# Optimization experiments

Hardware: AMD Instinct MI355X
Metric: run time of the kernel (lower is better)

Reference implementation:

```python
import jax, jax.numpy as jnp
import numpy as np

B, K, D = 32768, 8192, 1024
DECAY = 0.99
EPS = 1e-05
COMMIT = 0.25
NORM_EPS = 1e-12  # matches F.normalize eps


def _l2norm(x):
    n = jnp.linalg.norm(x, axis=-1, keepdims=True)
    return x / jnp.maximum(n, NORM_EPS)


def setup_inputs() -> dict:
    key = jax.random.key(0)
    k1, k2 = jax.random.split(key)
    z = jax.random.normal(k1, (B, D), jnp.float32)
    codebook = _l2norm(jax.random.normal(k2, (K, D), jnp.float32))
    ema_count = jnp.zeros((K,), jnp.float32)
    ema_weight = codebook  # init: ema_weight = codebook.clone()
    return {"z": z, "codebook": codebook, "ema_count": ema_count, "ema_weight": ema_weight}


def reference(z, codebook, ema_count, ema_weight):
    # cosine-similarity nearest-codeword search
    z_norm = _l2norm(z)                      # [B, D]
    cb_norm = _l2norm(codebook)              # [K, D]
    sim = jnp.einsum('bd,kd->bk', z_norm, cb_norm)  # [B, K]
    code_ids = jnp.argmax(sim, axis=-1)      # [B]
    q = codebook[code_ids]                   # [B, D] gather

    # EMA codebook update (training-mode statistics, no grad)
    zs = jax.lax.stop_gradient(z)
    n_k = jax.ops.segment_sum(jnp.ones((B,), z.dtype), code_ids, num_segments=K)  # [K]
    sum_k = jax.ops.segment_sum(zs, code_ids, num_segments=K)                      # [K, D]
    new_count = DECAY * ema_count + (1.0 - DECAY) * n_k
    new_weight = DECAY * ema_weight + (1.0 - DECAY) * sum_k
    new_codebook = new_weight / (new_count[:, None] + EPS)

    # commitment loss + straight-through estimator
    loss = COMMIT * jnp.mean((z - jax.lax.stop_gradient(q)) ** 2)
    z_q = z + jax.lax.stop_gradient(q - z)
    return z_q, code_ids, loss, new_codebook, new_count, new_weight
```

## Files before the change

kernel.cpp:

```cpp
#include <hip/hip_runtime.h>
#include <hip/hip_bf16.h>
#include <cstdint>
#include <cstddef>


#define B_N 32768
#define K_N 8192
#define D_N 1024
#define DECAYF 0.99f
#define OMDECAYF 0.01f
#define EPSF 1e-5f
#define NORM_EPSF 1e-12f

#define BT 128
#define KT 128
#define DT 32
#define LDT 40
#define NKT (K_N / KT)

typedef _Float16 f16x8 __attribute__((ext_vector_type(8)));
typedef _Float16 f16x4 __attribute__((ext_vector_type(4)));
typedef float f32x4 __attribute__((ext_vector_type(4)));

__global__ __launch_bounds__(256) void row_scale_kernel(
    const float* __restrict__ x, float* __restrict__ scale) {
  const int row = blockIdx.x;
  const float4 v =
      reinterpret_cast<const float4*>(x + (size_t)row * D_N)[threadIdx.x];
  float ss = v.x * v.x + v.y * v.y + v.z * v.z + v.w * v.w;
  for (int off = 32; off; off >>= 1) ss += __shfl_down(ss, off, 64);
  __shared__ float w[4];
  const int lane = threadIdx.x & 63, wid = threadIdx.x >> 6;
  if (lane == 0) w[wid] = ss;
  __syncthreads();
  if (threadIdx.x == 0) {
    const float t = w[0] + w[1] + w[2] + w[3];
    scale[row] = 64.0f / fmaxf(sqrtf(t), NORM_EPSF);
  }
}

__global__ __launch_bounds__(256) void gemm_argmax_kernel(
    const float* __restrict__ z, const float* __restrict__ cb,
    const float* __restrict__ scaleA, const float* __restrict__ scaleB,
    float* __restrict__ pval, int* __restrict__ pidx) {
  __shared__ _Float16 sAh[BT * LDT];
  __shared__ _Float16 sAl[BT * LDT];
  __shared__ _Float16 sBh[KT * LDT];
  __shared__ _Float16 sBl[KT * LDT];
  __shared__ float sSA[BT];
  __shared__ float sSB[KT];
  __shared__ float smv[BT][2];
  __shared__ int smc[BT][2];

  const int tid = threadIdx.x;
  const int kt = blockIdx.x & (NKT - 1);
  const int bt = blockIdx.x >> 6;
  const int b0 = bt * BT;
  const int k0 = kt * KT;

  if (tid < 128) sSA[tid] = scaleA[b0 + tid];
  else           sSB[tid - 128] = scaleB[k0 + tid - 128];
  __syncthreads();

  const int lane = tid & 63;
  const int q = lane >> 4;
  const int ln = lane & 15;
  const int wid = tid >> 6;
  const int wm = wid >> 1;
  const int wn = wid & 1;

  f32x4 acc[4][4];
#pragma unroll
  for (int i = 0; i < 4; ++i)
#pragma unroll
    for (int j = 0; j < 4; ++j) acc[i][j] = (f32x4){0.f, 0.f, 0.f, 0.f};

  for (int it = 0; it < D_N / DT; ++it) {
    const int d0 = it * DT;
#pragma unroll
    for (int c = 0; c < 4; ++c) {
      const int ch = tid + c * 256;
      const int row = ch >> 3;
      const int seg = (ch & 7) << 2;
      {
        float4 v = *reinterpret_cast<const float4*>(
            z + (size_t)(b0 + row) * D_N + d0 + seg);
        const float s = sSA[row];
        const float x0 = v.x * s, x1 = v.y * s, x2 = v.z * s, x3 = v.w * s;
        f16x4 h, l;
        h[0] = (_Float16)x0; l[0] = (_Float16)(x0 - (float)h[0]);
        h[1] = (_Float16)x1; l[1] = (_Float16)(x1 - (float)h[1]);
        h[2] = (_Float16)x2; l[2] = (_Float16)(x2 - (float)h[2]);
        h[3] = (_Float16)x3; l[3] = (_Float16)(x3 - (float)h[3]);
        *reinterpret_cast<f16x4*>(&sAh[row * LDT + seg]) = h;
        *reinterpret_cast<f16x4*>(&sAl[row * LDT + seg]) = l;
      }
      {
        float4 v = *reinterpret_cast<const float4*>(
            cb + (size_t)(k0 + row) * D_N + d0 + seg);
        const float s = sSB[row];
        const float x0 = v.x * s, x1 = v.y * s, x2 = v.z * s, x3 = v.w * s;
        f16x4 h, l;
        h[0] = (_Float16)x0; l[0] = (_Float16)(x0 - (float)h[0]);
        h[1] = (_Float16)x1; l[1] = (_Float16)(x1 - (float)h[1]);
        h[2] = (_Float16)x2; l[2] = (_Float16)(x2 - (float)h[2]);
        h[3] = (_Float16)x3; l[3] = (_Float16)(x3 - (float)h[3]);
        *reinterpret_cast<f16x4*>(&sBh[row * LDT + seg]) = h;
        *reinterpret_cast<f16x4*>(&sBl[row * LDT + seg]) = l;
      }
    }
    __syncthreads();

    f16x8 ah[4], al[4], bh[4], bl[4];
#pragma unroll
    for (int i = 0; i < 4; ++i) {
      const int r = wm * 64 + i * 16 + ln;
      ah[i] = *reinterpret_cast<const f16x8*>(&sAh[r * LDT + q * 8]);
      al[i] = *reinterpret_cast<const f16x8*>(&sAl[r * LDT + q * 8]);
    }
#pragma unroll
    for (int j = 0; j < 4; ++j) {
      const int r = wn * 64 + j * 16 + ln;
      bh[j] = *reinterpret_cast<const f16x8*>(&sBh[r * LDT + q * 8]);
      bl[j] = *reinterpret_cast<const f16x8*>(&sBl[r * LDT + q * 8]);
    }
#pragma unroll
    for (int i = 0; i < 4; ++i)
#pragma unroll
      for (int j = 0; j < 4; ++j) {
        acc[i][j] = __builtin_amdgcn_mfma_f32_16x16x32_f16(ah[i], bh[j],
                                                           acc[i][j], 0, 0, 0);
        acc[i][j] = __builtin_amdgcn_mfma_f32_16x16x32_f16(ah[i], bl[j],
                                                           acc[i][j], 0, 0, 0);
        acc[i][j] = __builtin_amdgcn_mfma_f32_16x16x32_f16(al[i], bh[j],
                                                           acc[i][j], 0, 0, 0);
      }
    __syncthreads();
  }

#pragma unroll
  for (int i = 0; i < 4; ++i) {
#pragma unroll
    for (int r = 0; r < 4; ++r) {
      float bv = -3.402823466e38f;
      int bc = 0;
#pragma unroll
      for (int j = 0; j < 4; ++j) {
        const float v = acc[i][j][r];
        const int c = wn * 64 + j * 16 + ln;
        if (v > bv) { bv = v; bc = c; }
      }
      for (int m = 1; m < 16; m <<= 1) {
        const float ov = __shfl_xor(bv, m, 16);
        const int oc = __shfl_xor(bc, m, 16);
        if (ov > bv || (ov == bv && oc < bc)) { bv = ov; bc = oc; }
      }
      if (ln == 0) {
        const int row = wm * 64 + i * 16 + q * 4 + r;
        smv[row][wn] = bv;
        smc[row][wn] = bc;
      }
    }
  }
  __syncthreads();
  if (tid < 128) {
    const float v0 = smv[tid][0], v1 = smv[tid][1];
    const int c0 = smc[tid][0], c1 = smc[tid][1];
    float bv; int bc;
    if (v1 > v0) { bv = v1; bc = c1; } else { bv = v0; bc = c0; }
    const size_t o = (size_t)kt * B_N + b0 + tid;
    pval[o] = bv;
    pidx[o] = k0 + bc;
  }
}

__global__ __launch_bounds__(256) void reduce_argmax_kernel(
    const float* __restrict__ pval, const int* __restrict__ pidx,
    int* __restrict__ ids, float* __restrict__ out_ids,
    float* __restrict__ counts) {
  const int b = blockIdx.x * 256 + threadIdx.x;
  float bv = -3.402823466e38f;
  int bc = 0;
  for (int kt = 0; kt < NKT; ++kt) {
    const float v = pval[(size_t)kt * B_N + b];
    if (v > bv) { bv = v; bc = pidx[(size_t)kt * B_N + b]; }
  }
  ids[b] = bc;
  out_ids[b] = (float)bc;
  atomicAdd(&counts[bc], 1.0f);
}

__global__ __launch_bounds__(256) void quant_scatter_kernel(
    const float* __restrict__ z, const float* __restrict__ cb,
    const int* __restrict__ ids, float* __restrict__ zq_out,
    float* __restrict__ sumk, double* __restrict__ loss_part) {
  double lsum = 0.0;
  const size_t total = (size_t)B_N * D_N;
  for (size_t idx = (size_t)blockIdx.x * 256 + threadIdx.x; idx < total;
       idx += (size_t)gridDim.x * 256) {
    const int b = (int)(idx >> 10);
    const int d = (int)(idx & 1023);
    const int id = ids[b];
    const float zv = z[idx];
    const float qv = cb[(size_t)id * D_N + d];
    const float t = qv - zv;
    zq_out[idx] = zv + t;
    const float df = zv - qv;
    const float sq = df * df;
    lsum += (double)sq;
    atomicAdd(&sumk[(size_t)id * D_N + d], zv);
  }
  for (int off = 32; off; off >>= 1) lsum += __shfl_down(lsum, off, 64);
  __shared__ double w[4];
  const int lane = threadIdx.x & 63, wid = threadIdx.x >> 6;
  if (lane == 0) w[wid] = lsum;
  __syncthreads();
  if (threadIdx.x == 0) loss_part[blockIdx.x] = w[0] + w[1] + w[2] + w[3];
}

__global__ __launch_bounds__(256) void finalize_kernel(
    const float* __restrict__ ema_count, const float* __restrict__ ema_weight,
    const float* __restrict__ counts, const float* __restrict__ sumk,
    float* __restrict__ out_codebook, float* __restrict__ out_count,
    float* __restrict__ out_weight) {
  const size_t idx = (size_t)blockIdx.x * 256 + threadIdx.x;
  const int k = (int)(idx >> 10);
  const float w = DECAYF * ema_weight[idx] + OMDECAYF * sumk[idx];
  const float nc = DECAYF * ema_count[k] + OMDECAYF * counts[k];
  out_weight[idx] = w;
  out_codebook[idx] = w / (nc + EPSF);
  if ((idx & 1023) == 0) out_count[k] = nc;
}

__global__ __launch_bounds__(256) void loss_kernel(
    const double* __restrict__ loss_part, float* __restrict__ out_loss, int n) {
  double s = 0.0;
  for (int i = threadIdx.x; i < n; i += 256) s += loss_part[i];
  for (int off = 32; off; off >>= 1) s += __shfl_down(s, off, 64);
  __shared__ double w[4];
  const int lane = threadIdx.x & 63, wid = threadIdx.x >> 6;
  if (lane == 0) w[wid] = s;
  __syncthreads();
  if (threadIdx.x == 0) {
    const double tot = w[0] + w[1] + w[2] + w[3];
    out_loss[0] = (float)(0.25 * (tot / (double)((size_t)B_N * D_N)));
  }
}

extern "C" void kernel_launch(void* const* d_in, const int* in_sizes, int n_in,
                              void* d_out, int out_size, void* d_ws,
                              size_t ws_size, hipStream_t stream) {
  const float* z = (const float*)d_in[0];
  const float* cb = (const float*)d_in[1];
  const float* ema_count = (const float*)d_in[2];
  const float* ema_weight = (const float*)d_in[3];
  float* out = (float*)d_out;

  const size_t o_zq = 0;
  const size_t o_ids = (size_t)B_N * D_N;
  const size_t o_loss = o_ids + B_N;
  const size_t o_cbk = o_loss + 1;
  const size_t o_cnt = o_cbk + (size_t)K_N * D_N;
  const size_t o_wt = o_cnt + K_N;

  char* ws = (char*)d_ws;
  float* scaleA = (float*)ws;
  float* scaleB = (float*)(ws + 131072);
  float* pval = (float*)(ws + 163840);
  int* pidx = (int*)(ws + 8552448);
  int* ids = (int*)(ws + 16941056);
  float* counts = (float*)(ws + 17072128);
  float* sumk = (float*)(ws + 17104896);
  double* loss_part = (double*)(ws + 50659328);

  row_scale_kernel<<<B_N, 256, 0, stream>>>(z, scaleA);
  row_scale_kernel<<<K_N, 256, 0, stream>>>(cb, scaleB);
  hipMemsetAsync(counts, 0, (size_t)K_N * sizeof(float), stream);
  hipMemsetAsync(sumk, 0, (size_t)K_N * D_N * sizeof(float), stream);

  gemm_argmax_kernel<<<(B_N / BT) * NKT, 256, 0, stream>>>(z, cb, scaleA,
                                                           scaleB, pval, pidx);
  reduce_argmax_kernel<<<B_N / 256, 256, 0, stream>>>(pval, pidx, ids,
                                                      out + o_ids, counts);
  quant_scatter_kernel<<<4096, 256, 0, stream>>>(z, cb, ids, out + o_zq, sumk,
                                                 loss_part);
  finalize_kernel<<<(K_N * D_N) / 256, 256, 0, stream>>>(
      ema_count, ema_weight, counts, sumk, out + o_cbk, out + o_cnt,
      out + o_wt);
  loss_kernel<<<1, 256, 0, stream>>>(loss_part, out + o_loss, 4096);
}
```

Before: 2.432 ms.

## Pre-split codebook into fp16 hi/lo tiles and stream via direct global-to-LDS loads

Adds a kernel that scales and splits the normalized codebook into fp16 high/low parts, stored in a tile-contiguous layout. The GEMM then loads B tiles straight into LDS with global_load_lds, so each block no longer converts the codebook itself. It also changes the LDS layout to a q-major unpadded form and sets launch bounds for occupancy. The cost is an extra pass over the codebook, extra workspace, and possible LDS bank conflicts now that the padding is gone.

```diff
diff --git a/kernel.cpp b/kernel.cpp
--- a/kernel.cpp
+++ b/kernel.cpp
@@ -15,12 +15,29 @@
 #define BT 128
 #define KT 128
 #define DT 32
-#define LDT 40
 #define NKT (K_N / KT)
+#define NIT (D_N / DT)
+#define TILE_HALVES 4096
 
 typedef _Float16 f16x8 __attribute__((ext_vector_type(8)));
-typedef _Float16 f16x4 __attribute__((ext_vector_type(4)));
 typedef float f32x4 __attribute__((ext_vector_type(4)));
+
+#define GLOAD_LDS16(gptr, lptr)                                         \
+  __builtin_amdgcn_global_load_lds(                                     \
+      (const __attribute__((address_space(1))) unsigned int*)(gptr),    \
+      (__attribute__((address_space(3))) unsigned int*)(lptr), 16, 0, 0)
+
+__device__ inline void split8(const float4 v0, const float4 v1, const float s,
+                              f16x8& h, f16x8& l) {
+  const float x[8] = {v0.x, v0.y, v0.z, v0.w, v1.x, v1.y, v1.z, v1.w};
+#pragma unroll
+  for (int k = 0; k < 8; ++k) {
+    const float xs = x[k] * s;
+    const _Float16 hh = (_Float16)xs;
+    h[k] = hh;
+    l[k] = (_Float16)(xs - (float)hh);
+  }
+}
 
 __global__ __launch_bounds__(256) void row_scale_kernel(
     const float* __restrict__ x, float* __restrict__ scale) {
@@ -39,16 +56,38 @@
   }
 }
 
-__global__ __launch_bounds__(256) void gemm_argmax_kernel(
-    const float* __restrict__ z, const float* __restrict__ cb,
-    const float* __restrict__ scaleA, const float* __restrict__ scaleB,
+__global__ __launch_bounds__(256) void split_cb_kernel(
+    const float* __restrict__ cb, const float* __restrict__ scale,
+    _Float16* __restrict__ cbh_t, _Float16* __restrict__ cbl_t) {
+  const int kt = blockIdx.x >> 5;
+  const int it = blockIdx.x & 31;
+  const int k0 = kt * KT;
+  const int d0 = it * DT;
+#pragma unroll
+  for (int c = 0; c < 2; ++c) {
+    const int p = threadIdx.x + c * 256;
+    const int q = p >> 7, r = p & 127;
+    const float s = scale[k0 + r];
+    const float* src = cb + (size_t)(k0 + r) * D_N + d0 + q * 8;
+    const float4 v0 = *reinterpret_cast<const float4*>(src);
+    const float4 v1 = *reinterpret_cast<const float4*>(src + 4);
+    f16x8 h, l;
+    split8(v0, v1, s, h, l);
+    const size_t o = ((size_t)blockIdx.x * 512 + p) * 8;
+    *reinterpret_cast<f16x8*>(cbh_t + o) = h;
+    *reinterpret_cast<f16x8*>(cbl_t + o) = l;
+  }
+}
+
+__global__ __launch_bounds__(256, 4) void gemm_argmax_kernel(
+    const float* __restrict__ z, const _Float16* __restrict__ cbh_t,
+    const _Float16* __restrict__ cbl_t, const float* __restrict__ scaleA,
     float* __restrict__ pval, int* __restrict__ pidx) {
-  __shared__ _Float16 sAh[BT * LDT];
-  __shared__ _Float16 sAl[BT * LDT];
-  __shared__ _Float16 sBh[KT * LDT];
-  __shared__ _Float16 sBl[KT * LDT];
+  __shared__ __align__(16) _Float16 sAh[TILE_HALVES];
+  __shared__ __align__(16) _Float16 sAl[TILE_HALVES];
+  __shared__ __align__(16) _Float16 sBh[TILE_HALVES];
+  __shared__ __align__(16) _Float16 sBl[TILE_HALVES];
   __shared__ float sSA[BT];
-  __shared__ float sSB[KT];
   __shared__ float smv[BT][2];
   __shared__ int smc[BT][2];
 
@@ -59,8 +98,6 @@
   const int k0 = kt * KT;
 
   if (tid < 128) sSA[tid] = scaleA[b0 + tid];
-  else           sSB[tid - 128] = scaleB[k0 + tid - 128];
-  __syncthreads();
 
   const int lane = tid & 63;
   const int q = lane >> 4;
@@ -69,60 +106,74 @@
   const int wm = wid >> 1;
   const int wn = wid & 1;
 
+  int aoff[4], boff[4];
+#pragma unroll
+  for (int i = 0; i < 4; ++i)
+    aoff[i] = ((q << 7) + wm * 64 + i * 16 + ln) * 8;
+#pragma unroll
+  for (int j = 0; j < 4; ++j)
+    boff[j] = ((q << 7) + wn * 64 + j * 16 + ln) * 8;
+
+  const int sq = tid & 3;
+  const int sr0 = tid >> 2;
+  const float* zp0 = z + (size_t)(b0 + sr0) * D_N + sq * 8;
+  const float* zp1 = z + (size_t)(b0 + sr0 + 64) * D_N + sq * 8;
+  const int aw0 = ((sq << 7) + sr0) * 8;
+  const int aw1 = ((sq << 7) + sr0 + 64) * 8;
+
+  const size_t bsrc = ((size_t)kt * NIT * 512 + wid * 128 + lane) * 8;
+  const _Float16* bh_base = cbh_t + bsrc;
+  const _Float16* bl_base = cbl_t + bsrc;
+  _Float16* ldsBh0 = &sBh[wid * 1024];
+  _Float16* ldsBh1 = &sBh[wid * 1024 + 512];
+  _Float16* ldsBl0 = &sBl[wid * 1024];
+  _Float16* ldsBl1 = &sBl[wid * 1024 + 512];
+
   f32x4 acc[4][4];
 #pragma unroll
   for (int i = 0; i < 4; ++i)
 #pragma unroll
     for (int j = 0; j < 4; ++j) acc[i][j] = (f32x4){0.f, 0.f, 0.f, 0.f};
 
-  for (int it = 0; it < D_N / DT; ++it) {
-    const int d0 = it * DT;
-#pragma unroll
-    for (int c = 0; c < 4; ++c) {
-      const int ch = tid + c * 256;
-      const int row = ch >> 3;
-      const int seg = (ch & 7) << 2;
-      {
-        float4 v = *reinterpret_cast<const float4*>(
-            z + (size_t)(b0 + row) * D_N + d0 + seg);
-        const float s = sSA[row];
-        const float x0 = v.x * s, x1 = v.y * s, x2 = v.z * s, x3 = v.w * s;
-        f16x4 h, l;
-        h[0] = (_Float16)x0; l[0] = (_Float16)(x0 - (float)h[0]);
-        h[1] = (_Float16)x1; l[1] = (_Float16)(x1 - (float)h[1]);
-        h[2] = (_Float16)x2; l[2] = (_Float16)(x2 - (float)h[2]);
-        h[3] = (_Float16)x3; l[3] = (_Float16)(x3 - (float)h[3]);
-        *reinterpret_cast<f16x4*>(&sAh[row * LDT + seg]) = h;
-        *reinterpret_cast<f16x4*>(&sAl[row * LDT + seg]) = l;
-      }
-      {
-        float4 v = *reinterpret_cast<const float4*>(
-            cb + (size_t)(k0 + row) * D_N + d0 + seg);
-        const float s = sSB[row];
-        const float x0 = v.x * s, x1 = v.y * s, x2 = v.z * s, x3 = v.w * s;
-        f16x4 h, l;
-        h[0] = (_Float16)x0; l[0] = (_Float16)(x0 - (float)h[0]);
-        h[1] = (_Float16)x1; l[1] = (_Float16)(x1 - (float)h[1]);
-        h[2] = (_Float16)x2; l[2] = (_Float16)(x2 - (float)h[2]);
-        h[3] = (_Float16)x3; l[3] = (_Float16)(x3 - (float)h[3]);
-        *reinterpret_cast<f16x4*>(&sBh[row * LDT + seg]) = h;
-        *reinterpret_cast<f16x4*>(&sBl[row * LDT + seg]) = l;
-      }
+  __syncthreads();
+
+  for (int it = 0; it < NIT; ++it) {
+    const size_t tb = (size_t)it * TILE_HALVES;
+    GLOAD_LDS16(bh_base + tb, ldsBh0);
+    GLOAD_LDS16(bh_base + tb + 512, ldsBh1);
+    GLOAD_LDS16(bl_base + tb, ldsBl0);
+    GLOAD_LDS16(bl_base + tb + 512, ldsBl1);
+
+    {
+      const float s0 = sSA[sr0];
+      const float4 v0 = *reinterpret_cast<const float4*>(zp0 + it * DT);
+      const float4 v1 = *reinterpret_cast<const float4*>(zp0 + it * DT + 4);
+      f16x8 h, l;
+      split8(v0, v1, s0, h, l);
+      *reinterpret_cast<f16x8*>(&sAh[aw0]) = h;
+      *reinterpret_cast<f16x8*>(&sAl[aw0]) = l;
+    }
+    {
+      const float s1 = sSA[sr0 + 64];
+      const float4 v0 = *reinterpret_cast<const float4*>(zp1 + it * DT);
+      const float4 v1 = *reinterpret_cast<const float4*>(zp1 + it * DT + 4);
+      f16x8 h, l;
+      split8(v0, v1, s1, h, l);
+      *reinterpret_cast<f16x8*>(&sAh[aw1]) = h;
+      *reinterpret_cast<f16x8*>(&sAl[aw1]) = l;
     }
     __syncthreads();
 
     f16x8 ah[4], al[4], bh[4], bl[4];
 #pragma unroll
     for (int i = 0; i < 4; ++i) {
-      const int r = wm * 64 + i * 16 + ln;
-      ah[i] = *reinterpret_cast<const f16x8*>(&sAh[r * LDT + q * 8]);
-      al[i] = *reinterpret_cast<const f16x8*>(&sAl[r * LDT + q * 8]);
+      ah[i] = *reinterpret_cast<const f16x8*>(&sAh[aoff[i]]);
+      al[i] = *reinterpret_cast<const f16x8*>(&sAl[aoff[i]]);
     }
 #pragma unroll
     for (int j = 0; j < 4; ++j) {
-      const int r = wn * 64 + j * 16 + ln;
-      bh[j] = *reinterpret_cast<const f16x8*>(&sBh[r * LDT + q * 8]);
-      bl[j] = *reinterpret_cast<const f16x8*>(&sBl[r * LDT + q * 8]);
+      bh[j] = *reinterpret_cast<const f16x8*>(&sBh[boff[j]]);
+      bl[j] = *reinterpret_cast<const f16x8*>(&sBl[boff[j]]);
     }
 #pragma unroll
     for (int i = 0; i < 4; ++i)
@@ -272,14 +323,17 @@
   float* counts = (float*)(ws + 17072128);
   float* sumk = (float*)(ws + 17104896);
   double* loss_part = (double*)(ws + 50659328);
+  _Float16* cbh_t = (_Float16*)(ws + 50692096);
+  _Float16* cbl_t = (_Float16*)(ws + 67469312);
 
   row_scale_kernel<<<B_N, 256, 0, stream>>>(z, scaleA);
   row_scale_kernel<<<K_N, 256, 0, stream>>>(cb, scaleB);
+  split_cb_kernel<<<NKT * NIT, 256, 0, stream>>>(cb, scaleB, cbh_t, cbl_t);
   hipMemsetAsync(counts, 0, (size_t)K_N * sizeof(float), stream);
   hipMemsetAsync(sumk, 0, (size_t)K_N * D_N * sizeof(float), stream);
 
-  gemm_argmax_kernel<<<(B_N / BT) * NKT, 256, 0, stream>>>(z, cb, scaleA,
-                                                           scaleB, pval, pidx);
+  gemm_argmax_kernel<<<(B_N / BT) * NKT, 256, 0, stream>>>(z, cbh_t, cbl_t,
+                                                           scaleA, pval, pidx);
   reduce_argmax_kernel<<<B_N / 256, 256, 0, stream>>>(pval, pidx, ids,
                                                       out + o_ids, counts);
   quant_scatter_kernel<<<4096, 256, 0, stream>>>(z, cb, ids, out + o_zq, sumk,
```

After: 2.045 ms. 1.19x faster.
